# Kernel tuning notes

Measured on AMD Instinct MI355X. Metric: run time of the kernel, lower is better.

## Reference

```python
import jax, jax.numpy as jnp
import numpy as np
from jax import lax

B, N, C = 16, 2304, 768
H_HEADS, D = 12, 64  # num_heads, head_dim
SCALE = 9.0 ** (-0.5)  # equivalent_head_dim ** -0.5


def setup_inputs() -> dict:
    key = jax.random.key(0)
    ks = jax.random.split(key, 8)
    return {
        "x": jax.random.normal(ks[0], (B, N, C), dtype=jnp.float32),
        "qkv_w": jax.random.normal(ks[1], (3 * C + 3 * D, C), dtype=jnp.float32) * 0.02,
        "qkv_b": jax.random.normal(ks[2], (3 * C + 3 * D,), dtype=jnp.float32) * 0.02,
        "w1": jax.random.normal(ks[3], (1, H_HEADS, D, D), dtype=jnp.float32) * 0.02,
        "w2": jax.random.normal(ks[4], (1, H_HEADS, D, D), dtype=jnp.float32) * 0.02,
        "w3": jax.random.normal(ks[5], (D, 1, 3, 3), dtype=jnp.float32) * 0.02,
        "proj_w": jax.random.normal(ks[6], (C, C + D), dtype=jnp.float32) * 0.02,
        "proj_b": jax.random.normal(ks[7], (C,), dtype=jnp.float32) * 0.02,
        "h": 48,
        "w": 48,
    }


def _inner_swiglu(k, v, w1, w2, lr=1.0):
    # k, v: [B, H, N, d]; w1, w2: [1, H, d, d]
    z1 = jnp.einsum('bhnd,hde->bhne', k, w1[0])
    z2 = jnp.einsum('bhnd,hde->bhne', k, w2[0])
    sig = jax.nn.sigmoid(z2)
    a = z2 * sig
    e = -v / float(v.shape[2]) * SCALE
    g1 = jnp.einsum('bhnd,bhne->bhde', k, e * a)
    g2 = jnp.einsum('bhnd,bhne->bhde', k, e * z1 * (sig * (1.0 + z2 * (1.0 - sig))))
    g1 = g1 / (jnp.linalg.norm(g1, axis=-2, keepdims=True) + 1.0)
    g2 = g2 / (jnp.linalg.norm(g2, axis=-2, keepdims=True) + 1.0)
    return w1 - lr * g1, w2 - lr * g2  # [B, H, d, d]


def _inner_3x3dwc(k, v, w3, hh, ww, lr=1.0):
    # k, v: [B, d, h, w]; w3: [d, 1, 3, 3]
    b, c = k.shape[0], k.shape[1]
    e = -v / float(hh * ww) * SCALE
    kp = jnp.pad(k, ((0, 0), (0, 0), (1, 1), (1, 1)))
    dots = []
    for ys in (0, 1, 2):  # 1 + dy
        for xs in (0, 1, 2):  # 1 + dx
            dots.append(jnp.sum(kp[:, :, ys:ys + hh, xs:xs + ww] * e, axis=(-2, -1)))
    g = jnp.stack(dots, axis=-1).reshape(b * c, 1, 3, 3)
    g = g / (jnp.sqrt(jnp.sum(g * g, axis=(-2, -1), keepdims=True)) + 1.0)
    return jnp.tile(w3, (b, 1, 1, 1)) - lr * g  # [B*d, 1, 3, 3]


def reference(x, qkv_w, qkv_b, w1, w2, w3, proj_w, proj_b, h, w):
    b, n, c = x.shape
    nh = w1.shape[1]
    d = c // nh
    qkv = x @ qkv_w.T + qkv_b  # [B, N, 3C + 3d]
    q1, k1, v1, q2, k2, v2 = jnp.split(
        qkv, [c, 2 * c, 3 * c, 3 * c + d, 3 * c + 2 * d], axis=-1)
    heads = lambda t: t.reshape(b, n, nh, d).transpose(0, 2, 1, 3)
    q1, k1, v1 = heads(q1), heads(k1), heads(v1)

    w1u, w2u = _inner_swiglu(k1, v1, w1, w2)
    x1 = jnp.einsum('bhnd,bhde->bhne', q1, w1u) * jax.nn.silu(
        jnp.einsum('bhnd,bhde->bhne', q1, w2u))
    x1 = x1.transpose(0, 2, 1, 3).reshape(b, n, c)

    spatial = lambda t: t.reshape(b, h, w, d).transpose(0, 3, 1, 2)  # [B, d, h, w]
    q2s, k2s, v2s = spatial(q2), spatial(k2), spatial(v2)
    w3u = _inner_3x3dwc(k2s, v2s, w3, h, w)
    x2 = lax.conv_general_dilated(
        q2s.reshape(1, b * d, h, w), w3u,
        window_strides=(1, 1), padding=((1, 1), (1, 1)),
        feature_group_count=b * d,
        dimension_numbers=('NCHW', 'OIHW', 'NCHW'))
    x2 = x2.reshape(b, d, n).transpose(0, 2, 1)  # [B, N, d]

    out = jnp.concatenate([x1, x2], axis=-1) @ proj_w.T + proj_b
    return out
```

## Files before the change

### kernel.cpp

```cpp
#include <hip/hip_runtime.h>
#include <hip/hip_bf16.h>
#include <math.h>

#define B_   16
#define N_   2304
#define C_   768
#define H_   12
#define D_   64
#define M_   (B_*N_)
#define NQKV 2496
#define NPAD 2560
#define CCP  832
#define LDW  76
#define EVS  (-1.0f/6912.0f)

typedef __bf16 bf16x8 __attribute__((ext_vector_type(8)));
typedef __bf16 bf16x4 __attribute__((ext_vector_type(4)));
typedef float  f32x4  __attribute__((ext_vector_type(4)));

static __device__ __forceinline__ void gload_lds16(const void* g, void* l) {
  __builtin_amdgcn_global_load_lds((const __attribute__((address_space(1))) void*)g,
                                   (__attribute__((address_space(3))) void*)l, 16, 0, 0);
}

static __device__ __forceinline__ bf16x8 ld8(const __bf16* p) {
  bf16x4 lo = *(const bf16x4*)p;
  bf16x4 hi = *(const bf16x4*)(p + 4);
  return __builtin_shufflevector(lo, hi, 0,1,2,3,4,5,6,7);
}

__global__ __launch_bounds__(256) void cvt_all(
    const float* __restrict__ x, const float* __restrict__ qkv_w,
    const float* __restrict__ qkv_b, const float* __restrict__ proj_w,
    __bf16* __restrict__ xb, __bf16* __restrict__ wqkvb,
    float* __restrict__ qkvbp, __bf16* __restrict__ pwb)
{
  const int blk = blockIdx.x;
  if (blk < 13824) {
    int i = blk * 256 + threadIdx.x;
    const float4* p = (const float4*)(x + (size_t)i * 8);
    float4 a = p[0], b = p[1];
    bf16x8 o = {(__bf16)a.x,(__bf16)a.y,(__bf16)a.z,(__bf16)a.w,
                (__bf16)b.x,(__bf16)b.y,(__bf16)b.z,(__bf16)b.w};
    *(bf16x8*)(xb + (size_t)i * 8) = o;
  } else if (blk < 14784) {
    int i = (blk - 13824) * 256 + threadIdx.x;
    int n = i / 96, c8 = i - n * 96;
    bf16x8 o;
    if (n < NQKV) {
      const float4* p = (const float4*)(qkv_w + (size_t)n * 768 + c8 * 8);
      float4 a = p[0], b = p[1];
      o = (bf16x8){(__bf16)a.x,(__bf16)a.y,(__bf16)a.z,(__bf16)a.w,
                   (__bf16)b.x,(__bf16)b.y,(__bf16)b.z,(__bf16)b.w};
    } else {
      o = (bf16x8){(__bf16)0.f,(__bf16)0.f,(__bf16)0.f,(__bf16)0.f,
                   (__bf16)0.f,(__bf16)0.f,(__bf16)0.f,(__bf16)0.f};
    }
    *(bf16x8*)(wqkvb + (size_t)n * 768 + c8 * 8) = o;
    if (i < NPAD) qkvbp[i] = (i < NQKV) ? qkv_b[i] : 0.0f;
  } else {
    int i = (blk - 14784) * 256 + threadIdx.x;
    if (i >= 79872) return;
    const float4* p = (const float4*)(proj_w + (size_t)i * 8);
    float4 a = p[0], b = p[1];
    bf16x8 o = {(__bf16)a.x,(__bf16)a.y,(__bf16)a.z,(__bf16)a.w,
                (__bf16)b.x,(__bf16)b.y,(__bf16)b.z,(__bf16)b.w};
    *(bf16x8*)(pwb + (size_t)i * 8) = o;
  }
}

template<int OUTF32>
__global__ __launch_bounds__(512, 2) void gemm8(
    const __bf16* __restrict__ A, const __bf16* __restrict__ Bt,
    const float* __restrict__ bias, void* __restrict__ Cout,
    const int K, const int ldc, const int nbn, const int KT)
{
  __shared__ __align__(16) __bf16 sA[2][2][128 * 64];
  __shared__ __align__(16) __bf16 sB[2][2][128 * 64];
  const int tid  = threadIdx.x;
  const int lane = tid & 63;
  const int wid  = tid >> 6;
  const int wm = wid >> 2;
  const int wn = wid & 3;
  const int l15 = lane & 15, lq = lane >> 4;

  const int nwg = gridDim.x;
  const int swz = ((int)blockIdx.x & 7) * (nwg >> 3) + ((int)blockIdx.x >> 3);
  const int bm = swz / nbn;
  const int bn = swz - bm * nbn;

  const int strow = tid >> 3;
  const int stoff = strow * 64 + (tid & 7) * 8;
  const __bf16* gA = A  + (size_t)((size_t)bm * 256 + strow) * K + ((tid & 7) ^ (strow & 7)) * 8;
  const __bf16* gB = Bt + (size_t)((size_t)bn * 256 + strow) * K + ((tid & 7) ^ (strow & 7)) * 8;

  f32x4 acc[2][4][2][2];
  #pragma unroll
  for (int a = 0; a < 2; ++a)
    #pragma unroll
    for (int m = 0; m < 4; ++m)
      #pragma unroll
      for (int b = 0; b < 2; ++b)
        #pragma unroll
        for (int n = 0; n < 2; ++n) acc[a][m][b][n] = (f32x4){0.f,0.f,0.f,0.f};

  bf16x8 af0[4][2], af1[4][2], bf0[2][2], bf1[2][2];

#define STAGE_A(q, h, T) do {                                                   \
    const size_t ko_ = (size_t)(T) * 64;                                        \
    gload_lds16(gA + (size_t)((h)*128 +  0) * K + ko_, &sA[q][h][stoff]);       \
    gload_lds16(gA + (size_t)((h)*128 + 64) * K + ko_, &sA[q][h][4096 + stoff]);\
  } while (0)
#define STAGE_B(q, h, T) do {                                                   \
    const size_t ko_ = (size_t)(T) * 64;                                        \
    gload_lds16(gB + (size_t)((h)*128 +  0) * K + ko_, &sB[q][h][stoff]);       \
    gload_lds16(gB + (size_t)((h)*128 + 64) * K + ko_, &sB[q][h][4096 + stoff]);\
  } while (0)
#define LOADA(DST, h, q) do {                                                   \
    _Pragma("unroll") for (int mf_ = 0; mf_ < 4; ++mf_) {                       \
      const int r_ = wm * 64 + mf_ * 16 + l15;                                  \
      _Pragma("unroll") for (int kk_ = 0; kk_ < 2; ++kk_)                       \
        DST[mf_][kk_] = *(const bf16x8*)&sA[q][h][r_ * 64 + (((kk_*4+lq) ^ (r_&7)) * 8)]; \
    } } while (0)
#define LOADB(DST, h, q) do {                                                   \
    _Pragma("unroll") for (int nf_ = 0; nf_ < 2; ++nf_) {                       \
      const int c_ = wn * 32 + nf_ * 16 + l15;                                  \
      _Pragma("unroll") for (int kk_ = 0; kk_ < 2; ++kk_)                       \
        DST[nf_][kk_] = *(const bf16x8*)&sB[q][h][c_ * 64 + (((kk_*4+lq) ^ (c_&7)) * 8)]; \
    } } while (0)
#define MMA(a_, b_, AF, BF) do {                                                \
    __builtin_amdgcn_s_setprio(1);                                              \
    _Pragma("unroll") for (int kk_ = 0; kk_ < 2; ++kk_)                         \
    _Pragma("unroll") for (int mf_ = 0; mf_ < 4; ++mf_)                         \
    _Pragma("unroll") for (int nf_ = 0; nf_ < 2; ++nf_)                         \
      acc[a_][mf_][b_][nf_] = __builtin_amdgcn_mfma_f32_16x16x32_bf16(          \
          AF[mf_][kk_], BF[nf_][kk_], acc[a_][mf_][b_][nf_], 0, 0, 0);          \
    __builtin_amdgcn_s_setprio(0);                                              \
  } while (0)
#define BAR  __builtin_amdgcn_s_barrier()
#define VMW4 asm volatile("s_waitcnt vmcnt(4)" ::: "memory")
#define VMW0 asm volatile("s_waitcnt vmcnt(0)" ::: "memory")

  STAGE_A(0, 0, 0); STAGE_A(0, 1, 0); STAGE_B(0, 0, 0); STAGE_B(0, 1, 0);
  STAGE_B(1, 0, 1);
  STAGE_A(1, 1, 1);
  VMW4;
  BAR;

  for (int t = 0; t + 1 < KT; t += 2) {
    LOADA(af0, 0, 0); LOADB(bf0, 0, 0);
    STAGE_A(1, 0, t + 1); STAGE_B(1, 1, t + 1);
    BAR; MMA(0, 0, af0, bf0); BAR;
    LOADA(af1, 1, 0);
    BAR; MMA(1, 0, af1, bf0); BAR;
    LOADB(bf1, 1, 0);
    if (t + 2 < KT) STAGE_B(0, 0, t + 2);
    BAR; MMA(1, 1, af1, bf1); BAR;
    if (t + 2 < KT) STAGE_A(0, 1, t + 2);
    BAR; MMA(0, 1, af0, bf1);
    if (t + 2 < KT) { VMW4; } else { VMW0; }
    BAR;
    LOADA(af0, 0, 1); LOADB(bf0, 0, 1);
    if (t + 2 < KT) { STAGE_A(0, 0, t + 2); STAGE_B(0, 1, t + 2); }
    BAR; MMA(0, 0, af0, bf0); BAR;
    LOADA(af1, 1, 1);
    BAR; MMA(1, 0, af1, bf0); BAR;
    LOADB(bf1, 1, 1);
    if (t + 3 < KT) STAGE_B(1, 0, t + 3);
    BAR; MMA(1, 1, af1, bf1); BAR;
    if (t + 3 < KT) STAGE_A(1, 1, t + 3);
    BAR; MMA(0, 1, af0, bf1);
    if (t + 3 < KT) { VMW4; } else { VMW0; }
    BAR;
  }
  if (KT & 1) {
    LOADA(af0, 0, 0); LOADB(bf0, 0, 0);
    MMA(0, 0, af0, bf0);
    LOADA(af1, 1, 0);
    MMA(1, 0, af1, bf0);
    LOADB(bf1, 1, 0);
    MMA(1, 1, af1, bf1);
    MMA(0, 1, af0, bf1);
  }
#undef STAGE_A
#undef STAGE_B
#undef LOADA
#undef LOADB
#undef MMA

  #pragma unroll
  for (int b = 0; b < 2; ++b)
    #pragma unroll
    for (int nf = 0; nf < 2; ++nf) {
      const int col = bn * 256 + b * 128 + wn * 32 + nf * 16 + l15;
      const float bs = bias[col];
      #pragma unroll
      for (int a = 0; a < 2; ++a)
        #pragma unroll
        for (int mf = 0; mf < 4; ++mf) {
          const int row0 = bm * 256 + a * 128 + wm * 64 + mf * 16 + lq * 4;
          #pragma unroll
          for (int r = 0; r < 4; ++r) {
            float v = acc[a][mf][b][nf][r] + bs;
            if (OUTF32) ((float*)Cout)[(size_t)(row0 + r) * ldc + col] = v;
            else        ((__bf16*)Cout)[(size_t)(row0 + r) * ldc + col] = (__bf16)v;
          }
        }
    }
}

__global__ __launch_bounds__(256, 3) void grad_combo(
    const __bf16* __restrict__ qkv, const float* __restrict__ w1,
    const float* __restrict__ w2, float* __restrict__ gpart,
    float* __restrict__ w3p)
{
  __shared__ union U {
    struct { __bf16 w1T[64 * LDW], w2T[64 * LDW], kNt1[64 * LDW],
                    kT[64 * LDW], t2T[64 * LDW]; } ig;
    struct { __bf16 kS[6 * 50 * 64]; float red[4][9][64]; } dg;
  } u;
  const int tid = threadIdx.x;

  if (blockIdx.x < 768) {
    const int blk = blockIdx.x;
    const int bh = blk >> 2, seg = blk & 3;
    const int b = bh / H_, h = bh - b * H_;
    const int wid = tid >> 6, lane = tid & 63;
    const int wr = wid >> 1, wc = wid & 1, l15 = lane & 15, lq = lane >> 4;

    const float4* w1p4 = (const float4*)(w1 + h * 4096);
    const float4* w2p4 = (const float4*)(w2 + h * 4096);
    #pragma unroll
    for (int it = 0; it < 4; ++it) {
      int i4 = tid + it * 256;
      float4 a = w1p4[i4], c = w2p4[i4];
      int d = i4 >> 4, e0 = (i4 * 4) & 63;
      u.ig.w1T[(e0+0)*LDW+d] = (__bf16)a.x; u.ig.w1T[(e0+1)*LDW+d] = (__bf16)a.y;
      u.ig.w1T[(e0+2)*LDW+d] = (__bf16)a.z; u.ig.w1T[(e0+3)*LDW+d] = (__bf16)a.w;
      u.ig.w2T[(e0+0)*LDW+d] = (__bf16)c.x; u.ig.w2T[(e0+1)*LDW+d] = (__bf16)c.y;
      u.ig.w2T[(e0+2)*LDW+d] = (__bf16)c.z; u.ig.w2T[(e0+3)*LDW+d] = (__bf16)c.w;
    }

    f32x4 g1a[2][2], g2a[2][2];
    #pragma unroll
    for (int i = 0; i < 2; ++i)
      #pragma unroll
      for (int j = 0; j < 2; ++j) { g1a[i][j] = (f32x4){0.f,0.f,0.f,0.f}; g2a[i][j] = (f32x4){0.f,0.f,0.f,0.f}; }

    const size_t rowb = (size_t)b * N_;
    const int koff = C_ + h * D_;
    const int voff = 2 * C_ + h * D_;
    const int sn = tid >> 2, sdb = tid & 3;
    __syncthreads();

    for (int ci = 0; ci < 9; ++ci) {
      const int n0 = seg * 576 + ci * 64;
      {
        const __bf16* src = qkv + (rowb + n0 + sn) * (size_t)NPAD + koff + sdb * 16;
        bf16x8 va = *(const bf16x8*)src;
        bf16x8 vb = *(const bf16x8*)(src + 8);
        __bf16* kn = &u.ig.kNt1[sn * LDW + sdb * 16];
        *(bf16x4*)(kn + 0)  = __builtin_shufflevector(va, va, 0,1,2,3);
        *(bf16x4*)(kn + 4)  = __builtin_shufflevector(va, va, 4,5,6,7);
        *(bf16x4*)(kn + 8)  = __builtin_shufflevector(vb, vb, 0,1,2,3);
        *(bf16x4*)(kn + 12) = __builtin_shufflevector(vb, vb, 4,5,6,7);
        #pragma unroll
        for (int j = 0; j < 8; ++j) u.ig.kT[(sdb * 16 + j) * LDW + sn] = va[j];
        #pragma unroll
        for (int j = 0; j < 8; ++j) u.ig.kT[(sdb * 16 + 8 + j) * LDW + sn] = vb[j];
      }

      float vv[2][2][4];
      #pragma unroll
      for (int mi = 0; mi < 2; ++mi)
        #pragma unroll
        for (int ni = 0; ni < 2; ++ni) {
          int nl = wr * 32 + mi * 16 + lq * 4;
          int e  = wc * 32 + ni * 16 + l15;
          const __bf16* vp = qkv + (rowb + n0 + nl) * (size_t)NPAD + voff + e;
          #pragma unroll
          for (int r = 0; r < 4; ++r) vv[mi][ni][r] = (float)vp[(size_t)r * NPAD];
        }
      __syncthreads();

      f32x4 z1[2][2], z2[2][2];
      #pragma unroll
      for (int i = 0; i < 2; ++i)
        #pragma unroll
        for (int j = 0; j < 2; ++j) { z1[i][j] = (f32x4){0.f,0.f,0.f,0.f}; z2[i][j] = (f32x4){0.f,0.f,0.f,0.f}; }
      #pragma unroll
      for (int kk = 0; kk < 2; ++kk) {
        bf16x8 af[2], b1[2], b2[2];
        #pragma unroll
        for (int mi = 0; mi < 2; ++mi)
          af[mi] = ld8(&u.ig.kNt1[(wr * 32 + mi * 16 + l15) * LDW + kk * 32 + lq * 8]);
        #pragma unroll
        for (int ni = 0; ni < 2; ++ni) {
          int e = wc * 32 + ni * 16 + l15;
          b1[ni] = ld8(&u.ig.w1T[e * LDW + kk * 32 + lq * 8]);
          b2[ni] = ld8(&u.ig.w2T[e * LDW + kk * 32 + lq * 8]);
        }
        #pragma unroll
        for (int mi = 0; mi < 2; ++mi)
          #pragma unroll
          for (int ni = 0; ni < 2; ++ni) {
            z1[mi][ni] = __builtin_amdgcn_mfma_f32_16x16x32_bf16(af[mi], b1[ni], z1[mi][ni], 0, 0, 0);
            z2[mi][ni] = __builtin_amdgcn_mfma_f32_16x16x32_bf16(af[mi], b2[ni], z2[mi][ni], 0, 0, 0);
          }
      }
      __syncthreads();

      #pragma unroll
      for (int mi = 0; mi < 2; ++mi)
        #pragma unroll
        for (int ni = 0; ni < 2; ++ni) {
          int nl = wr * 32 + mi * 16 + lq * 4;
          int e  = wc * 32 + ni * 16 + l15;
          #pragma unroll
          for (int r = 0; r < 4; ++r) {
            float ev  = vv[mi][ni][r] * EVS;
            float z1v = z1[mi][ni][r], z2v = z2[mi][ni][r];
            float sg  = 1.0f / (1.0f + __expf(-z2v));
            float t1  = ev * (z2v * sg);
            float t2  = ev * z1v * (sg * (1.0f + z2v * (1.0f - sg)));
            u.ig.kNt1[e * LDW + nl + r] = (__bf16)t1;
            u.ig.t2T [e * LDW + nl + r] = (__bf16)t2;
          }
        }
      __syncthreads();

      #pragma unroll
      for (int kk = 0; kk < 2; ++kk) {
        bf16x8 af[2], b1[2], b2[2];
        #pragma unroll
        for (int mi = 0; mi < 2; ++mi)
          af[mi] = ld8(&u.ig.kT[(wr * 32 + mi * 16 + l15) * LDW + kk * 32 + lq * 8]);
        #pragma unroll
        for (int ni = 0; ni < 2; ++ni) {
          int e = wc * 32 + ni * 16 + l15;
          b1[ni] = ld8(&u.ig.kNt1[e * LDW + kk * 32 + lq * 8]);
          b2[ni] = ld8(&u.ig.t2T [e * LDW + kk * 32 + lq * 8]);
        }
        #pragma unroll
        for (int mi = 0; mi < 2; ++mi)
          #pragma unroll
          for (int ni = 0; ni < 2; ++ni) {
            g1a[mi][ni] = __builtin_amdgcn_mfma_f32_16x16x32_bf16(af[mi], b1[ni], g1a[mi][ni], 0, 0, 0);
            g2a[mi][ni] = __builtin_amdgcn_mfma_f32_16x16x32_bf16(af[mi], b2[ni], g2a[mi][ni], 0, 0, 0);
          }
      }
      __syncthreads();
    }

    float* gp = gpart + (size_t)blk * 8192;
    #pragma unroll
    for (int mi = 0; mi < 2; ++mi)
      #pragma unroll
      for (int ni = 0; ni < 2; ++ni)
        #pragma unroll
        for (int r = 0; r < 4; ++r) {
          int d = wr * 32 + mi * 16 + lq * 4 + r;
          int e = wc * 32 + ni * 16 + l15;
          gp[d * 64 + e]        = g1a[mi][ni][r];
          gp[4096 + d * 64 + e] = g2a[mi][ni][r];
        }
  } else {
    const int blk = blockIdx.x - 768;
    const int b = blk / 12, sp = blk - b * 12;
    const int dd = tid & 63, rl = tid >> 6;
    for (int i = tid; i < 9600; i += 256) ((unsigned*)u.dg.kS)[i] = 0u;
    __syncthreads();
    const size_t base = (size_t)b * N_ * NPAD;
    for (int i = tid; i < 6 * 48 * 8; i += 256) {
      int y6 = i / 384; int rem = i - y6 * 384; int x = rem >> 3; int c8 = rem & 7;
      int y = 4 * sp - 1 + y6;
      if (y >= 0 && y < 48) {
        int p = y * 48 + x;
        bf16x8 v = *(const bf16x8*)&qkv[base + (size_t)p * NPAD + 2368 + c8 * 8];
        *(bf16x8*)&u.dg.kS[((y6 * 50) + x + 1) * 64 + c8 * 8] = v;
      }
    }
    __syncthreads();
    float acc[9];
    #pragma unroll
    for (int j = 0; j < 9; ++j) acc[j] = 0.f;
    const int y = 4 * sp + rl;
    for (int x = 0; x < 48; ++x) {
      int p = y * 48 + x;
      float e = (float)qkv[base + (size_t)p * NPAD + 2432 + dd] * EVS;
      #pragma unroll
      for (int j = 0; j < 9; ++j) {
        int ys = j / 3, xs = j - ys * 3;
        acc[j] += (float)u.dg.kS[((rl + ys) * 50 + x + xs) * 64 + dd] * e;
      }
    }
    #pragma unroll
    for (int j = 0; j < 9; ++j) u.dg.red[rl][j][dd] = acc[j];
    __syncthreads();
    if (rl == 0) {
      #pragma unroll
      for (int j = 0; j < 9; ++j) {
        float s = u.dg.red[0][j][dd] + u.dg.red[1][j][dd]
                + u.dg.red[2][j][dd] + u.dg.red[3][j][dd];
        w3p[((size_t)(b * 12 + sp) * 64 + dd) * 9 + j] = s;
      }
    }
  }
}

__global__ __launch_bounds__(256) void inner_upd(
    const float* __restrict__ gpart, const float* __restrict__ w1,
    const float* __restrict__ w2, __bf16* __restrict__ wu)
{
  const int bh = blockIdx.x;
  const int h = bh % H_;
  const int tid = threadIdx.x;
  __shared__ float g1[64 * 65], g2[64 * 65];
  __shared__ float nrm1[64], nrm2[64];
  const float* w1p = w1 + h * 4096;
  const float* w2p = w2 + h * 4096;

  for (int idx = tid; idx < 4096; idx += 256) {
    float s1 = 0.f, s2 = 0.f;
    #pragma unroll
    for (int s = 0; s < 4; ++s) {
      const float* gp = gpart + (size_t)(bh * 4 + s) * 8192;
      s1 += gp[idx]; s2 += gp[4096 + idx];
    }
    int d = idx >> 6, e = idx & 63;
    g1[d * 65 + e] = s1; g2[d * 65 + e] = s2;
  }
  __syncthreads();
  if (tid < 128) {
    const float* gs = (tid < 64) ? g1 : g2;
    int e = tid & 63;
    float s = 0.f;
    for (int d = 0; d < 64; ++d) { float gv = gs[d * 65 + e]; s += gv * gv; }
    float rn = 1.0f / (sqrtf(s) + 1.0f);
    if (tid < 64) nrm1[e] = rn; else nrm2[e] = rn;
  }
  __syncthreads();
  __bf16* wub = wu + (size_t)bh * 8192;
  for (int idx = tid; idx < 4096; idx += 256) {
    int d = idx >> 6, e = idx & 63;
    wub[idx]        = (__bf16)(w1p[idx] - g1[d * 65 + e] * nrm1[e]);
    wub[4096 + idx] = (__bf16)(w2p[idx] - g2[d * 65 + e] * nrm2[e]);
  }
}

__global__ __launch_bounds__(256) void apply_combo(
    const __bf16* __restrict__ qkv, const __bf16* __restrict__ wu,
    const float* __restrict__ w3p, const float* __restrict__ w3,
    __bf16* __restrict__ concat)
{
  __shared__ union U {
    struct { __bf16 w1T[64 * LDW], w2T[64 * LDW], qN[64 * LDW]; } ia;
    struct { __bf16 qS[6 * 50 * 64]; } da;
  } u;
  const int tid = threadIdx.x;

  if (blockIdx.x >= 192) {
    const int blk = blockIdx.x - 192;
    const int bh = blk / 6, seg = blk - bh * 6;
    const int b = bh / H_, h = bh - b * H_;
    const int wid = tid >> 6, lane = tid & 63;
    const int wr = wid >> 1, wc = wid & 1, l15 = lane & 15, lq = lane >> 4;

    const bf16x8* wub8 = (const bf16x8*)(wu + (size_t)bh * 8192);
    #pragma unroll
    for (int it = 0; it < 2; ++it) {
      int i8 = tid + it * 256;
      bf16x8 a = wub8[i8], c = wub8[512 + i8];
      int d = i8 >> 3, e0 = (i8 & 7) * 8;
      #pragma unroll
      for (int j = 0; j < 8; ++j) {
        u.ia.w1T[(e0+j)*LDW+d] = a[j];
        u.ia.w2T[(e0+j)*LDW+d] = c[j];
      }
    }

    const size_t rowb = (size_t)b * N_;
    const int qoff = h * D_;
    const int sn = tid >> 2, sdb = tid & 3;

    for (int ci = 0; ci < 6; ++ci) {
      const int n0 = seg * 384 + ci * 64;
      {
        const __bf16* src = qkv + (rowb + n0 + sn) * (size_t)NPAD + qoff + sdb * 16;
        bf16x8 va = *(const bf16x8*)src;
        bf16x8 vb = *(const bf16x8*)(src + 8);
        __bf16* kn = &u.ia.qN[sn * LDW + sdb * 16];
        *(bf16x4*)(kn + 0)  = __builtin_shufflevector(va, va, 0,1,2,3);
        *(bf16x4*)(kn + 4)  = __builtin_shufflevector(va, va, 4,5,6,7);
        *(bf16x4*)(kn + 8)  = __builtin_shufflevector(vb, vb, 0,1,2,3);
        *(bf16x4*)(kn + 12) = __builtin_shufflevector(vb, vb, 4,5,6,7);
      }
      __syncthreads();
      f32x4 y1[2][2], y2[2][2];
      #pragma unroll
      for (int i = 0; i < 2; ++i)
        #pragma unroll
        for (int j = 0; j < 2; ++j) { y1[i][j] = (f32x4){0.f,0.f,0.f,0.f}; y2[i][j] = (f32x4){0.f,0.f,0.f,0.f}; }
      #pragma unroll
      for (int kk = 0; kk < 2; ++kk) {
        bf16x8 af[2], b1[2], b2[2];
        #pragma unroll
        for (int mi = 0; mi < 2; ++mi)
          af[mi] = ld8(&u.ia.qN[(wr * 32 + mi * 16 + l15) * LDW + kk * 32 + lq * 8]);
        #pragma unroll
        for (int ni = 0; ni < 2; ++ni) {
          int e = wc * 32 + ni * 16 + l15;
          b1[ni] = ld8(&u.ia.w1T[e * LDW + kk * 32 + lq * 8]);
          b2[ni] = ld8(&u.ia.w2T[e * LDW + kk * 32 + lq * 8]);
        }
        #pragma unroll
        for (int mi = 0; mi < 2; ++mi)
          #pragma unroll
          for (int ni = 0; ni < 2; ++ni) {
            y1[mi][ni] = __builtin_amdgcn_mfma_f32_16x16x32_bf16(af[mi], b1[ni], y1[mi][ni], 0, 0, 0);
            y2[mi][ni] = __builtin_amdgcn_mfma_f32_16x16x32_bf16(af[mi], b2[ni], y2[mi][ni], 0, 0, 0);
          }
      }
      #pragma unroll
      for (int mi = 0; mi < 2; ++mi)
        #pragma unroll
        for (int ni = 0; ni < 2; ++ni) {
          int nl = wr * 32 + mi * 16 + lq * 4;
          int e  = wc * 32 + ni * 16 + l15;
          #pragma unroll
          for (int r = 0; r < 4; ++r) {
            float a1 = y1[mi][ni][r], a2 = y2[mi][ni][r];
            float sg = 1.0f / (1.0f + __expf(-a2));
            concat[(rowb + n0 + nl + r) * (size_t)CCP + h * D_ + e] = (__bf16)(a1 * (a2 * sg));
          }
        }
      __syncthreads();
    }
  } else {
    const int blk = blockIdx.x;
    const int b = blk / 12, sp = blk - b * 12;
    const int dd = tid & 63, rl = tid >> 6;
    for (int i = tid; i < 9600; i += 256) ((unsigned*)u.da.qS)[i] = 0u;
    __syncthreads();
    const size_t base = (size_t)b * N_ * NPAD;
    for (int i = tid; i < 6 * 48 * 8; i += 256) {
      int y6 = i / 384; int rem = i - y6 * 384; int x = rem >> 3; int c8 = rem & 7;
      int y = 4 * sp - 1 + y6;
      if (y >= 0 && y < 48) {
        int p = y * 48 + x;
        bf16x8 v = *(const bf16x8*)&qkv[base + (size_t)p * NPAD + 2304 + c8 * 8];
        *(bf16x8*)&u.da.qS[((y6 * 50) + x + 1) * 64 + c8 * 8] = v;
      }
    }
    float g[9];
    #pragma unroll
    for (int j = 0; j < 9; ++j) g[j] = 0.f;
    for (int s = 0; s < 12; ++s)
      #pragma unroll
      for (int j = 0; j < 9; ++j)
        g[j] += w3p[((size_t)(b * 12 + s) * 64 + dd) * 9 + j];
    float ss = 0.f;
    #pragma unroll
    for (int j = 0; j < 9; ++j) ss += g[j] * g[j];
    float rn = 1.0f / (sqrtf(ss) + 1.0f);
    float wv[9];
    #pragma unroll
    for (int j = 0; j < 9; ++j) wv[j] = w3[dd * 9 + j] - g[j] * rn;
    __syncthreads();
    const int y = 4 * sp + rl;
    for (int x = 0; x < 48; ++x) {
      float s = 0.f;
      #pragma unroll
      for (int j = 0; j < 9; ++j) {
        int ys = j / 3, xs = j - ys * 3;
        s += (float)u.da.qS[((rl + ys) * 50 + x + xs) * 64 + dd] * wv[j];
      }
      int p = y * 48 + x;
      concat[((size_t)b * N_ + p) * CCP + 768 + dd] = (__bf16)s;
    }
  }
}

extern "C" void kernel_launch(void* const* d_in, const int* in_sizes, int n_in,
                              void* d_out, int out_size, void* d_ws, size_t ws_size,
                              hipStream_t stream) {
  const float* x      = (const float*)d_in[0];
  const float* qkv_w  = (const float*)d_in[1];
  const float* qkv_b  = (const float*)d_in[2];
  const float* w1     = (const float*)d_in[3];
  const float* w2     = (const float*)d_in[4];
  const float* w3     = (const float*)d_in[5];
  const float* proj_w = (const float*)d_in[6];
  const float* proj_b = (const float*)d_in[7];

  char* ws = (char*)d_ws;
  __bf16* xb     = (__bf16*)ws;
  __bf16* wqkvb  = (__bf16*)(ws + 56623104);
  float*  qkvbp  = (float*) (ws + 60555264);
  __bf16* concat = (__bf16*)ws;
  __bf16* qkvb16 = (__bf16*)(ws + 66060288);
  __bf16* pwb    = (__bf16*)(ws + 254803968);
  float*  w3p    = (float*) (ws + 256217088);
  float*  gpart  = (float*) (ws + 256659456);
  __bf16* wu     = (__bf16*)(ws + 281825280);

  cvt_all<<<15096, 256, 0, stream>>>(x, qkv_w, qkv_b, proj_w, xb, wqkvb, qkvbp, pwb);

  gemm8<0><<<1440, 512, 0, stream>>>(xb, wqkvb, qkvbp, (void*)qkvb16,
                                     768, NPAD, 10, 12);

  grad_combo <<< 960, 256, 0, stream>>>(qkvb16, w1, w2, gpart, w3p);
  inner_upd  <<< 192, 256, 0, stream>>>(gpart, w1, w2, wu);
  apply_combo<<<1344, 256, 0, stream>>>(qkvb16, wu, w3p, w3, concat);

  gemm8<1><<<432, 512, 0, stream>>>(concat, pwb, proj_b, d_out,
                                    832, 768, 3, 13);
}
```

Before: 393.9 us.

## Fuse fp32-to-bf16 conversion of x into the QKV GEMM A-tile load

Removes the separate pass that converts x from fp32 to bf16 in the workspace. The new QKV GEMM kernel reads fp32 x directly into registers, converts it to bf16 and writes it into swizzled LDS, while the weights still stream through global_load_lds. This avoids writing and re-reading a 56MB bf16 copy of x. In exchange the GEMM reads twice the A bytes per tile, needs more registers (launch bounds drop to 1 block per CU) and pipelines the A tile through registers instead of asynchronous LDS loads.

```diff
diff --git a/kernel.cpp b/kernel.cpp
--- a/kernel.cpp
+++ b/kernel.cpp
@@ -30,21 +30,13 @@
 }
 
 __global__ __launch_bounds__(256) void cvt_all(
-    const float* __restrict__ x, const float* __restrict__ qkv_w,
-    const float* __restrict__ qkv_b, const float* __restrict__ proj_w,
-    __bf16* __restrict__ xb, __bf16* __restrict__ wqkvb,
-    float* __restrict__ qkvbp, __bf16* __restrict__ pwb)
+    const float* __restrict__ qkv_w, const float* __restrict__ qkv_b,
+    const float* __restrict__ proj_w,
+    __bf16* __restrict__ wqkvb, float* __restrict__ qkvbp, __bf16* __restrict__ pwb)
 {
   const int blk = blockIdx.x;
-  if (blk < 13824) {
+  if (blk < 960) {
     int i = blk * 256 + threadIdx.x;
-    const float4* p = (const float4*)(x + (size_t)i * 8);
-    float4 a = p[0], b = p[1];
-    bf16x8 o = {(__bf16)a.x,(__bf16)a.y,(__bf16)a.z,(__bf16)a.w,
-                (__bf16)b.x,(__bf16)b.y,(__bf16)b.z,(__bf16)b.w};
-    *(bf16x8*)(xb + (size_t)i * 8) = o;
-  } else if (blk < 14784) {
-    int i = (blk - 13824) * 256 + threadIdx.x;
     int n = i / 96, c8 = i - n * 96;
     bf16x8 o;
     if (n < NQKV) {
@@ -59,7 +51,7 @@
     *(bf16x8*)(wqkvb + (size_t)n * 768 + c8 * 8) = o;
     if (i < NPAD) qkvbp[i] = (i < NQKV) ? qkv_b[i] : 0.0f;
   } else {
-    int i = (blk - 14784) * 256 + threadIdx.x;
+    int i = (blk - 960) * 256 + threadIdx.x;
     if (i >= 79872) return;
     const float4* p = (const float4*)(proj_w + (size_t)i * 8);
     float4 a = p[0], b = p[1];
@@ -67,6 +59,134 @@
                 (__bf16)b.x,(__bf16)b.y,(__bf16)b.z,(__bf16)b.w};
     *(bf16x8*)(pwb + (size_t)i * 8) = o;
   }
+}
+
+__global__ __launch_bounds__(512, 1) void gemmXF(
+    const float* __restrict__ A, const __bf16* __restrict__ Bt,
+    const float* __restrict__ bias, __bf16* __restrict__ Cout,
+    const int K, const int ldc, const int nbn, const int KT)
+{
+  __shared__ __align__(16) __bf16 sA[2][256 * 64];
+  __shared__ __align__(16) __bf16 sB[2][256 * 64];
+  const int tid  = threadIdx.x;
+  const int lane = tid & 63;
+  const int wid  = tid >> 6;
+  const int wm = wid >> 2;
+  const int wn = wid & 3;
+  const int l15 = lane & 15, lq = lane >> 4;
+
+  const int nwg = gridDim.x;
+  const int swz = ((int)blockIdx.x & 7) * (nwg >> 3) + ((int)blockIdx.x >> 3);
+  const int bm = swz / nbn;
+  const int bn = swz - bm * nbn;
+
+  const int strow  = tid >> 3;
+  const int stoff  = strow * 64 + (tid & 7) * 8;
+  const int schunk = ((tid & 7) ^ (strow & 7)) * 8;
+  const float*  gA = A  + (size_t)((size_t)bm * 256 + strow) * K + schunk;
+  const __bf16* gB = Bt + (size_t)((size_t)bn * 256 + strow) * K + schunk;
+
+  f32x4 acc[2][4][2][2];
+  #pragma unroll
+  for (int a = 0; a < 2; ++a)
+    #pragma unroll
+    for (int m = 0; m < 4; ++m)
+      #pragma unroll
+      for (int b = 0; b < 2; ++b)
+        #pragma unroll
+        for (int n = 0; n < 2; ++n) acc[a][m][b][n] = (f32x4){0.f,0.f,0.f,0.f};
+
+  float4 av[4][2];
+  bf16x8 af0[4][2], af1[4][2], bf0[2][2], bf1[2][2];
+
+#define A_ISSUE(T) do {                                                         \
+    const size_t ko_ = (size_t)(T) * 64;                                        \
+    _Pragma("unroll") for (int j_ = 0; j_ < 4; ++j_) {                          \
+      const float* ap_ = gA + (size_t)(j_ * 64) * K + ko_;                      \
+      av[j_][0] = *(const float4*)(ap_);                                        \
+      av[j_][1] = *(const float4*)(ap_ + 4);                                    \
+    } } while (0)
+#define A_WRITE(q) do {                                                         \
+    _Pragma("unroll") for (int j_ = 0; j_ < 4; ++j_) {                          \
+      bf16x8 o_ = {(__bf16)av[j_][0].x,(__bf16)av[j_][0].y,                     \
+                   (__bf16)av[j_][0].z,(__bf16)av[j_][0].w,                     \
+                   (__bf16)av[j_][1].x,(__bf16)av[j_][1].y,                     \
+                   (__bf16)av[j_][1].z,(__bf16)av[j_][1].w};                    \
+      *(bf16x8*)&sA[q][j_ * 4096 + stoff] = o_;                                 \
+    } } while (0)
+#define B_STAGE(q, T) do {                                                      \
+    const size_t ko_ = (size_t)(T) * 64;                                        \
+    _Pragma("unroll") for (int j_ = 0; j_ < 4; ++j_)                            \
+      gload_lds16(gB + (size_t)(j_ * 64) * K + ko_, &sB[q][j_ * 4096 + stoff]); \
+  } while (0)
+#define LOADA(DST, h, q) do {                                                   \
+    _Pragma("unroll") for (int mf_ = 0; mf_ < 4; ++mf_) {                       \
+      const int r_ = (h) * 128 + wm * 64 + mf_ * 16 + l15;                      \
+      _Pragma("unroll") for (int kk_ = 0; kk_ < 2; ++kk_)                       \
+        DST[mf_][kk_] = *(const bf16x8*)&sA[q][r_ * 64 + (((kk_*4+lq) ^ (r_&7)) * 8)]; \
+    } } while (0)
+#define LOADB(DST, h, q) do {                                                   \
+    _Pragma("unroll") for (int nf_ = 0; nf_ < 2; ++nf_) {                       \
+      const int c_ = (h) * 128 + wn * 32 + nf_ * 16 + l15;                      \
+      _Pragma("unroll") for (int kk_ = 0; kk_ < 2; ++kk_)                       \
+        DST[nf_][kk_] = *(const bf16x8*)&sB[q][c_ * 64 + (((kk_*4+lq) ^ (c_&7)) * 8)]; \
+    } } while (0)
+#define MMA(a_, b_, AF, BF) do {                                                \
+    __builtin_amdgcn_s_setprio(1);                                              \
+    _Pragma("unroll") for (int kk_ = 0; kk_ < 2; ++kk_)                         \
+    _Pragma("unroll") for (int mf_ = 0; mf_ < 4; ++mf_)                         \
+    _Pragma("unroll") for (int nf_ = 0; nf_ < 2; ++nf_)                         \
+      acc[a_][mf_][b_][nf_] = __builtin_amdgcn_mfma_f32_16x16x32_bf16(          \
+          AF[mf_][kk_], BF[nf_][kk_], acc[a_][mf_][b_][nf_], 0, 0, 0);          \
+    __builtin_amdgcn_s_setprio(0);                                              \
+  } while (0)
+
+  A_ISSUE(0);
+  B_STAGE(0, 0);
+  A_WRITE(0);
+  __syncthreads();
+
+  for (int t = 0; t < KT; ++t) {
+    const int q = t & 1;
+    if (t + 1 < KT) {
+      A_ISSUE(t + 1);
+      B_STAGE(q ^ 1, t + 1);
+    }
+
+    LOADB(bf0, 0, q); LOADB(bf1, 1, q);
+    LOADA(af0, 0, q);
+    MMA(0, 0, af0, bf0); MMA(0, 1, af0, bf1);
+    LOADA(af1, 1, q);
+    MMA(1, 0, af1, bf0); MMA(1, 1, af1, bf1);
+
+    if (t + 1 < KT) {
+      A_WRITE(q ^ 1);
+      __syncthreads();
+    }
+  }
+#undef A_ISSUE
+#undef A_WRITE
+#undef B_STAGE
+#undef LOADA
+#undef LOADB
+#undef MMA
+
+  #pragma unroll
+  for (int b = 0; b < 2; ++b)
+    #pragma unroll
+    for (int nf = 0; nf < 2; ++nf) {
+      const int col = bn * 256 + b * 128 + wn * 32 + nf * 16 + l15;
+      const float bs = bias[col];
+      #pragma unroll
+      for (int a = 0; a < 2; ++a)
+        #pragma unroll
+        for (int mf = 0; mf < 4; ++mf) {
+          const int row0 = bm * 256 + a * 128 + wm * 64 + mf * 16 + lq * 4;
+          #pragma unroll
+          for (int r = 0; r < 4; ++r)
+            Cout[(size_t)(row0 + r) * ldc + col] = (__bf16)(acc[a][mf][b][nf][r] + bs);
+        }
+    }
 }
 
 template<int OUTF32>
@@ -594,7 +714,6 @@
   const float* proj_b = (const float*)d_in[7];
 
   char* ws = (char*)d_ws;
-  __bf16* xb     = (__bf16*)ws;
   __bf16* wqkvb  = (__bf16*)(ws + 56623104);
   float*  qkvbp  = (float*) (ws + 60555264);
   __bf16* concat = (__bf16*)ws;
@@ -604,10 +723,10 @@
   float*  gpart  = (float*) (ws + 256659456);
   __bf16* wu     = (__bf16*)(ws + 281825280);
 
-  cvt_all<<<15096, 256, 0, stream>>>(x, qkv_w, qkv_b, proj_w, xb, wqkvb, qkvbp, pwb);
-
-  gemm8<0><<<1440, 512, 0, stream>>>(xb, wqkvb, qkvbp, (void*)qkvb16,
-                                     768, NPAD, 10, 12);
+  cvt_all<<<1272, 256, 0, stream>>>(qkv_w, qkv_b, proj_w, wqkvb, qkvbp, pwb);
+
+  gemmXF<<<1440, 512, 0, stream>>>(x, wqkvb, qkvbp, qkvb16,
+                                   768, NPAD, 10, 12);
 
   grad_combo <<< 960, 256, 0, stream>>>(qkvb16, w1, w2, gpart, w3p);
   inner_upd  <<< 192, 256, 0, stream>>>(gpart, w1, w2, wu);
```

Measured after the change: 419.7 us. 6.6% more time.
